# Optimization experiments

Hardware: AMD Instinct MI355X
Metric: run time of the kernel (lower is better)

The kernel has to match this reference:

```python
import jax, jax.numpy as jnp
import numpy as np

C = 128          # hidden_channels
H = 8            # num_heads
D = C // H       # head dim = 16
OUT = 64         # out_channels
L = 2            # num_layers
NN = (30000, 60000, 6000)                 # poi, road, region node counts
NE = (200000, 300000, 200000, 100000)     # edges per edge type
ETS = ((0, 1), (1, 1), (1, 2), (2, 0))    # (src_type, dst_type) per edge type


def setup_inputs():
    key = jax.random.key(0)
    ks = iter(jax.random.split(key, 40))
    s = 1.0 / np.sqrt(C)
    sd = 1.0 / np.sqrt(D)
    inp = {}
    inp['x_poi'] = jax.random.normal(next(ks), (NN[0], C), jnp.float32)
    inp['x_road'] = jax.random.normal(next(ks), (NN[1], C), jnp.float32)
    inp['x_region'] = jax.random.normal(next(ks), (NN[2], C), jnp.float32)
    for et, (si, di) in enumerate(ETS):
        inp[f'e{et}_src'] = jax.random.randint(next(ks), (NE[et],), 0, NN[si], jnp.int32)
        inp[f'e{et}_dst'] = jax.random.randint(next(ks), (NE[et],), 0, NN[di], jnp.int32)
    # per-node-type input projection
    inp['lin_w'] = jax.random.normal(next(ks), (3, C, C), jnp.float32) * s
    inp['lin_b'] = jax.random.normal(next(ks), (3, C), jnp.float32) * 0.01
    # per-layer, per-node-type K/Q/V and output projections
    for nm in ('kw', 'qw', 'vw', 'aw'):
        inp[nm] = jax.random.normal(next(ks), (L, 3, C, C), jnp.float32) * s
    for nm in ('kb', 'qb', 'vb', 'ab'):
        inp[nm] = jax.random.normal(next(ks), (L, 3, C), jnp.float32) * 0.01
    # per-layer, per-edge-type relation matrices and priors
    inp['a_rel'] = jax.random.normal(next(ks), (L, 4, H, D, D), jnp.float32) * sd
    inp['m_rel'] = jax.random.normal(next(ks), (L, 4, H, D, D), jnp.float32) * sd
    inp['p_rel'] = jnp.ones((L, 4, H), jnp.float32)
    inp['skip'] = jnp.ones((L, 3), jnp.float32)
    inp['out_w'] = jax.random.normal(next(ks), (C, OUT), jnp.float32) * s
    inp['out_b'] = jnp.zeros((OUT,), jnp.float32)
    return inp


def _seg_softmax(alpha, dst, n):
    amax = jax.lax.stop_gradient(jax.ops.segment_max(alpha, dst, num_segments=n))
    ex = jnp.exp(alpha - amax[dst])
    den = jax.ops.segment_sum(ex, dst, num_segments=n)
    return ex / (den[dst] + 1e-16)


def _hgt_forward(xs, edges, lin_w, lin_b, kw, kb, qw, qb, vw, vb, aw, ab,
                 a_rel, m_rel, p_rel, skip, out_w, out_b):
    # per-node-type input linear + relu
    xs = [jax.nn.relu(xs[i] @ lin_w[i] + lin_b[i]) for i in range(3)]
    scale = 1.0 / np.sqrt(D)
    for l in range(L):
        k = [(xs[i] @ kw[l, i] + kb[l, i]).reshape(-1, H, D) for i in range(3)]
        q = [(xs[i] @ qw[l, i] + qb[l, i]).reshape(-1, H, D) for i in range(3)]
        v = [(xs[i] @ vw[l, i] + vb[l, i]).reshape(-1, H, D) for i in range(3)]
        agg = [jnp.zeros((NN[i], H, D), xs[i].dtype) for i in range(3)]
        for et, (si, di) in enumerate(ETS):
            src, dst = edges[et]
            n = NN[di]
            ke = jnp.einsum('ehd,hdf->ehf', k[si][src], a_rel[l, et])   # [E,H,D]
            alpha = jnp.einsum('ehd,ehd->eh', q[di][dst], ke) * p_rel[l, et] * scale
            alpha = _seg_softmax(alpha, dst, n)                          # [E,H]
            m = jnp.einsum('ehd,hdf->ehf', v[si][src], m_rel[l, et])    # [E,H,D]
            agg[di] = agg[di] + jax.ops.segment_sum(m * alpha[..., None], dst, num_segments=n)
        new_xs = []
        for i in range(3):
            o = jax.nn.gelu(agg[i].reshape(-1, C)) @ aw[l, i] + ab[l, i]
            beta = jax.nn.sigmoid(skip[l, i])
            o = beta * o + (1.0 - beta) * xs[i]
            new_xs.append(jax.nn.relu(o))  # HGT applies activation after each conv
        xs = new_xs
    return (xs[0] @ out_w + out_b, xs[1] @ out_w + out_b, xs[2] @ out_w + out_b)


def reference(x_poi, x_road, x_region,
              e0_src, e0_dst, e1_src, e1_dst, e2_src, e2_dst, e3_src, e3_dst,
              lin_w, lin_b, kw, kb, qw, qb, vw, vb, aw, ab,
              a_rel, m_rel, p_rel, skip, out_w, out_b):
    edges = ((e0_src, e0_dst), (e1_src, e1_dst), (e2_src, e2_dst), (e3_src, e3_dst))
    return _hgt_forward([x_poi, x_road, x_region], edges,
                        lin_w, lin_b, kw, kb, qw, qb, vw, vb, aw, ab,
                        a_rel, m_rel, p_rel, skip, out_w, out_b)
```

## Files before the change

### kernel.cpp

```cpp
#include <hip/hip_runtime.h>
#include <cstddef>
#include <cstdint>


typedef __attribute__((ext_vector_type(8))) short short8;
typedef __attribute__((ext_vector_type(4))) float floatx4;

__device__ __forceinline__ float gelu_fast(float x) {
    float u = 1.5957691216057308f * x * (1.0f + 0.044715f * x * x);
    return x / (1.0f + __expf(-u));
}

__device__ __forceinline__ unsigned short f2bf(float f) {
    unsigned u = __float_as_uint(f);
    u += 0x7fffu + ((u >> 16) & 1);
    return (unsigned short)(u >> 16);
}

__device__ __forceinline__ float bf2f(unsigned short h) {
    return __uint_as_float((unsigned)h << 16);
}

__device__ __forceinline__ void up8(uint4 u, float* f) {
    f[0] = __uint_as_float(u.x << 16); f[1] = __uint_as_float(u.x & 0xffff0000u);
    f[2] = __uint_as_float(u.y << 16); f[3] = __uint_as_float(u.y & 0xffff0000u);
    f[4] = __uint_as_float(u.z << 16); f[5] = __uint_as_float(u.z & 0xffff0000u);
    f[6] = __uint_as_float(u.w << 16); f[7] = __uint_as_float(u.w & 0xffff0000u);
}

__device__ __forceinline__ uint4 pk8(const float* f) {
    uint4 u;
    u.x = (unsigned)f2bf(f[0]) | ((unsigned)f2bf(f[1]) << 16);
    u.y = (unsigned)f2bf(f[2]) | ((unsigned)f2bf(f[3]) << 16);
    u.z = (unsigned)f2bf(f[4]) | ((unsigned)f2bf(f[5]) << 16);
    u.w = (unsigned)f2bf(f[6]) | ((unsigned)f2bf(f[7]) << 16);
    return u;
}

__global__ __launch_bounds__(256, 2) void gemm_proj_all(
    const unsigned short* __restrict__ xs_bf,
    const unsigned short* __restrict__ Wl,
    const float* __restrict__ bl,
    unsigned short* __restrict__ proj)
{
    const int    NN_[3]  = {30000, 60000, 6000};
    const int    NPAN[3] = {469, 938, 94};
    const int    OFFr[3] = {0, 30000, 90000};
    const int    WOFF[3] = {0, 49152, 131072};
    const int    BOFF[3] = {0, 384, 1024};
    const size_t POFF[3] = {0, 11520000u, 49920000u};
    const int    LDO[3]  = {384, 640, 384};

    int b = blockIdx.x, t, cp, rb;
    if (b < 590)      { t = 1; cp = b / 118; rb = b - cp * 118; }
    else if (b < 767) { int lb = b - 590; t = 0; cp = lb / 59; rb = lb - cp * 59; }
    else              { int lb = b - 767; t = 2; cp = lb / 12; rb = lb - cp * 12; }
    int p0 = rb * 8, p1 = p0 + 8;
    if (p1 > NPAN[t]) p1 = NPAN[t];

    const unsigned short* Abf = xs_bf + (size_t)OFFr[t] * 128;
    const unsigned short* Wt  = Wl + WOFF[t];
    const float* bias = bl + BOFF[t] + cp * 128;
    unsigned short* outbf = proj + POFF[t];
    const int ldo = LDO[t], Nrows = NN_[t];

    const int wave = threadIdx.x >> 6, lane = threadIdx.x & 63;
    const int quad = lane >> 4, l16 = lane & 15;

    short8 B[2][4][4];
    {
        const unsigned short* wb = Wt + (size_t)(cp * 128 + l16) * 128 + quad * 8;
        #pragma unroll
        for (int T = 0; T < 2; ++T)
            #pragma unroll
            for (int c = 0; c < 4; ++c)
                #pragma unroll
                for (int kc = 0; kc < 4; ++kc)
                    B[T][c][kc] = *(const short8*)(wb + (size_t)(T * 64 + c * 16) * 128 + kc * 32);
    }
    float4 bv[2][4];
    #pragma unroll
    for (int T = 0; T < 2; ++T)
        #pragma unroll
        for (int c = 0; c < 4; ++c)
            bv[T][c] = *(const float4*)(bias + T * 64 + c * 16 + quad * 4);

    short8 Acur[4];
    {
        int m = p0 * 64 + wave * 16 + l16; if (m >= Nrows) m = Nrows - 1;
        const unsigned short* ap = Abf + (size_t)m * 128 + quad * 8;
        #pragma unroll
        for (int kc = 0; kc < 4; ++kc) Acur[kc] = *(const short8*)(ap + kc * 32);
    }
    for (int p = p0; p < p1; ++p) {
        short8 Anx[4];
        {
            int m = (p + 1) * 64 + wave * 16 + l16; if (m >= Nrows) m = Nrows - 1;
            const unsigned short* ap = Abf + (size_t)m * 128 + quad * 8;
            #pragma unroll
            for (int kc = 0; kc < 4; ++kc) Anx[kc] = *(const short8*)(ap + kc * 32);
        }
        floatx4 acc[2][4];
        #pragma unroll
        for (int T = 0; T < 2; ++T)
            #pragma unroll
            for (int c = 0; c < 4; ++c) acc[T][c] = (floatx4){0.f, 0.f, 0.f, 0.f};
        #pragma unroll
        for (int kc = 0; kc < 4; ++kc)
            #pragma unroll
            for (int T = 0; T < 2; ++T)
                #pragma unroll
                for (int c = 0; c < 4; ++c)
                    acc[T][c] = __builtin_amdgcn_mfma_f32_16x16x32_bf16(B[T][c][kc], Acur[kc], acc[T][c], 0, 0, 0);
        int node = p * 64 + wave * 16 + l16;
        if (node < Nrows) {
            unsigned short* op = outbf + (size_t)node * ldo + cp * 128 + quad * 4;
            #pragma unroll
            for (int T = 0; T < 2; ++T)
                #pragma unroll
                for (int c = 0; c < 4; ++c) {
                    uint2 u;
                    u.x = (unsigned)f2bf(acc[T][c][0] + bv[T][c].x) |
                          ((unsigned)f2bf(acc[T][c][1] + bv[T][c].y) << 16);
                    u.y = (unsigned)f2bf(acc[T][c][2] + bv[T][c].z) |
                          ((unsigned)f2bf(acc[T][c][3] + bv[T][c].w) << 16);
                    *(uint2*)(op + T * 64 + c * 16) = u;
                }
        }
        #pragma unroll
        for (int kc = 0; kc < 4; ++kc) Acur[kc] = Anx[kc];
    }
}

template<bool AF32, bool GIN, bool SKIP>
__global__ __launch_bounds__(256, 2) void gemm_node(
    const void* __restrict__ a0v, const void* __restrict__ a1v, const void* __restrict__ a2v,
    const unsigned short* __restrict__ WtB, const float* __restrict__ biasB,
    const unsigned short* __restrict__ xoldB, const float* __restrict__ skipB,
    unsigned short* __restrict__ outB)
{
    const int TN[3]   = {30000, 60000, 6000};
    const int NPAN[3] = {469, 938, 94};
    const int TOFF[3] = {0, 30000, 90000};
    int b = blockIdx.x, t, rb;
    if (b < 235)      { t = 0; rb = b; }
    else if (b < 704) { t = 1; rb = b - 235; }
    else              { t = 2; rb = b - 704; }
    int p0 = rb * 2, p1 = p0 + 2;
    if (p1 > NPAN[t]) p1 = NPAN[t];
    int Nrows = TN[t];
    const void* av = (t == 0) ? a0v : (t == 1) ? a1v : a2v;
    const unsigned short* xold = xoldB + (size_t)TOFF[t] * 128;
    unsigned short* out = outB + (size_t)TOFF[t] * 128;

    const int wave = threadIdx.x >> 6, lane = threadIdx.x & 63;
    const int quad = lane >> 4, l16 = lane & 15;

    short8 B[8][4];
    {
        const unsigned short* wb = WtB + (size_t)t * 16384 + (size_t)l16 * 128 + quad * 8;
        #pragma unroll
        for (int c = 0; c < 8; ++c)
            #pragma unroll
            for (int kc = 0; kc < 4; ++kc)
                B[c][kc] = *(const short8*)(wb + (size_t)c * 2048 + kc * 32);
    }
    float beta = 0.f, omb = 0.f;
    if (SKIP) { beta = 1.0f / (1.0f + __expf(-skipB[t])); omb = 1.0f - beta; }

    short8 Acur[4];
    {
        int m = p0 * 64 + wave * 16 + l16; if (m >= Nrows) m = Nrows - 1;
        size_t base = (size_t)m * 128 + quad * 8;
        #pragma unroll
        for (int kc = 0; kc < 4; ++kc) {
            if (AF32) {
                const float* ap = (const float*)av + base;
                float4 f0 = *(const float4*)(ap + kc * 32);
                float4 f1 = *(const float4*)(ap + kc * 32 + 4);
                float af[8] = {f0.x, f0.y, f0.z, f0.w, f1.x, f1.y, f1.z, f1.w};
                short8 a;
                #pragma unroll
                for (int i = 0; i < 8; ++i) a[i] = (short)f2bf(af[i]);
                Acur[kc] = a;
            } else if (GIN) {
                const unsigned short* ap = (const unsigned short*)av + base;
                short8 a8 = *(const short8*)(ap + kc * 32);
                short8 a;
                #pragma unroll
                for (int i = 0; i < 8; ++i)
                    a[i] = (short)f2bf(gelu_fast(bf2f((unsigned short)a8[i])));
                Acur[kc] = a;
            } else {
                const unsigned short* ap = (const unsigned short*)av + base;
                Acur[kc] = *(const short8*)(ap + kc * 32);
            }
        }
    }
    for (int p = p0; p < p1; ++p) {
        float4 Fnx[4][2];
        short8 Snx[4];
        {
            int m = (p + 1) * 64 + wave * 16 + l16; if (m >= Nrows) m = Nrows - 1;
            size_t base = (size_t)m * 128 + quad * 8;
            #pragma unroll
            for (int kc = 0; kc < 4; ++kc) {
                if (AF32) {
                    const float* ap = (const float*)av + base;
                    Fnx[kc][0] = *(const float4*)(ap + kc * 32);
                    Fnx[kc][1] = *(const float4*)(ap + kc * 32 + 4);
                } else {
                    const unsigned short* ap = (const unsigned short*)av + base;
                    Snx[kc] = *(const short8*)(ap + kc * 32);
                }
            }
        }
        int node = p * 64 + wave * 16 + l16;
        int ncl = (node < Nrows) ? node : (Nrows - 1);
        uint2 xo[8];
        if (SKIP) {
            #pragma unroll
            for (int c = 0; c < 8; ++c)
                xo[c] = *(const uint2*)(xold + (size_t)ncl * 128 + c * 16 + quad * 4);
        }
        floatx4 acc[8];
        #pragma unroll
        for (int c = 0; c < 8; ++c) acc[c] = (floatx4){0.f, 0.f, 0.f, 0.f};
        #pragma unroll
        for (int kc = 0; kc < 4; ++kc)
            #pragma unroll
            for (int c = 0; c < 8; ++c)
                acc[c] = __builtin_amdgcn_mfma_f32_16x16x32_bf16(B[c][kc], Acur[kc], acc[c], 0, 0, 0);
        if (node < Nrows) {
            #pragma unroll
            for (int c = 0; c < 8; ++c) {
                int col0 = c * 16 + quad * 4;
                float4 bv = *(const float4*)(biasB + t * 128 + col0);
                float o0 = acc[c][0] + bv.x, o1 = acc[c][1] + bv.y;
                float o2 = acc[c][2] + bv.z, o3 = acc[c][3] + bv.w;
                if (SKIP) {
                    o0 = beta * o0 + omb * __uint_as_float(xo[c].x << 16);
                    o1 = beta * o1 + omb * __uint_as_float(xo[c].x & 0xffff0000u);
                    o2 = beta * o2 + omb * __uint_as_float(xo[c].y << 16);
                    o3 = beta * o3 + omb * __uint_as_float(xo[c].y & 0xffff0000u);
                }
                o0 = fmaxf(o0, 0.f); o1 = fmaxf(o1, 0.f);
                o2 = fmaxf(o2, 0.f); o3 = fmaxf(o3, 0.f);
                uint2 u;
                u.x = (unsigned)f2bf(o0) | ((unsigned)f2bf(o1) << 16);
                u.y = (unsigned)f2bf(o2) | ((unsigned)f2bf(o3) << 16);
                *(uint2*)(out + (size_t)node * 128 + col0) = u;
            }
        }
        #pragma unroll
        for (int kc = 0; kc < 4; ++kc) {
            if (AF32) {
                float af[8] = {Fnx[kc][0].x, Fnx[kc][0].y, Fnx[kc][0].z, Fnx[kc][0].w,
                               Fnx[kc][1].x, Fnx[kc][1].y, Fnx[kc][1].z, Fnx[kc][1].w};
                short8 a;
                #pragma unroll
                for (int i = 0; i < 8; ++i) a[i] = (short)f2bf(af[i]);
                Acur[kc] = a;
            } else if (GIN) {
                short8 a;
                #pragma unroll
                for (int i = 0; i < 8; ++i)
                    a[i] = (short)f2bf(gelu_fast(bf2f((unsigned short)Snx[kc][i])));
                Acur[kc] = a;
            } else {
                Acur[kc] = Snx[kc];
            }
        }
    }
}

__global__ __launch_bounds__(256, 3) void gemm_out(
    const unsigned short* __restrict__ Abf,
    const unsigned short* __restrict__ Wt,
    const float* __restrict__ bias,
    float* __restrict__ out, int Nrows)
{
    const int wave = threadIdx.x >> 6, lane = threadIdx.x & 63;
    const int quad = lane >> 4, l16 = lane & 15;
    int p0 = blockIdx.x * 4, p1 = p0 + 4;

    short8 B[4][4];
    {
        const unsigned short* wb = Wt + (size_t)l16 * 128 + quad * 8;
        #pragma unroll
        for (int c = 0; c < 4; ++c)
            #pragma unroll
            for (int kc = 0; kc < 4; ++kc)
                B[c][kc] = *(const short8*)(wb + (size_t)c * 2048 + kc * 32);
    }
    float4 bv[4];
    #pragma unroll
    for (int c = 0; c < 4; ++c) bv[c] = *(const float4*)(bias + c * 16 + quad * 4);

    short8 Acur[4];
    {
        int m = p0 * 64 + wave * 16 + l16; if (m >= Nrows) m = Nrows - 1;
        const unsigned short* ap = Abf + (size_t)m * 128 + quad * 8;
        #pragma unroll
        for (int kc = 0; kc < 4; ++kc) Acur[kc] = *(const short8*)(ap + kc * 32);
    }
    for (int p = p0; p < p1; ++p) {
        short8 Anx[4];
        {
            int m = (p + 1) * 64 + wave * 16 + l16; if (m >= Nrows) m = Nrows - 1;
            const unsigned short* ap = Abf + (size_t)m * 128 + quad * 8;
            #pragma unroll
            for (int kc = 0; kc < 4; ++kc) Anx[kc] = *(const short8*)(ap + kc * 32);
        }
        floatx4 acc[4];
        #pragma unroll
        for (int c = 0; c < 4; ++c) acc[c] = (floatx4){0.f, 0.f, 0.f, 0.f};
        #pragma unroll
        for (int kc = 0; kc < 4; ++kc)
            #pragma unroll
            for (int c = 0; c < 4; ++c)
                acc[c] = __builtin_amdgcn_mfma_f32_16x16x32_bf16(B[c][kc], Acur[kc], acc[c], 0, 0, 0);
        int node = p * 64 + wave * 16 + l16;
        if (node < Nrows) {
            #pragma unroll
            for (int c = 0; c < 4; ++c) {
                float4 o;
                o.x = acc[c][0] + bv[c].x; o.y = acc[c][1] + bv[c].y;
                o.z = acc[c][2] + bv[c].z; o.w = acc[c][3] + bv[c].w;
                *(float4*)(out + (size_t)node * 64 + c * 16 + quad * 4) = o;
            }
        }
        #pragma unroll
        for (int kc = 0; kc < 4; ++kc) Acur[kc] = Anx[kc];
    }
}

__global__ __launch_bounds__(128) void prep_qpack(
    const float* __restrict__ qw, const float* __restrict__ qb,
    unsigned short* __restrict__ Wpack, float* __restrict__ bpack)
{
    const int pre[3] = {0, 49152, 131072};
    const int preB[3] = {0, 384, 1024};
    int n = threadIdx.x, k = blockIdx.x, t = blockIdx.y, l = blockIdx.z;
    unsigned short* Wp = Wpack + (size_t)l * 180224 + pre[t];
    Wp[(size_t)n * 128 + k] = f2bf(qw[(size_t)(l * 3 + t) * 16384 + (size_t)k * 128 + n]);
    if (k == 0) bpack[l * 1408 + preB[t] + n] = qb[(l * 3 + t) * 128 + n];
}

__global__ __launch_bounds__(128) void fold_rel_pack(
    const float* __restrict__ kw, const float* __restrict__ kb,
    const float* __restrict__ vw, const float* __restrict__ vb,
    const float* __restrict__ a_rel, const float* __restrict__ m_rel,
    unsigned short* __restrict__ Wpack, float* __restrict__ bpack)
{
    const int SIv[4] = {0, 1, 1, 2};
    const int SLOT[4] = {0, 0, 1, 0};
    const int pre[3] = {0, 49152, 131072};
    const int preB[3] = {0, 384, 1024};
    int hf = threadIdx.x, h = hf >> 4, f = hf & 15;
    int c = blockIdx.x, et = blockIdx.y, l = blockIdx.z;
    int si = SIv[et];
    const float* kwp  = kw + (size_t)(l * 3 + si) * 16384;
    const float* vwp  = vw + (size_t)(l * 3 + si) * 16384;
    const float* kbp  = kb + (size_t)(l * 3 + si) * 128;
    const float* vbp  = vb + (size_t)(l * 3 + si) * 128;
    const float* arel = a_rel + (size_t)(l * 4 + et) * 2048;
    const float* mrel = m_rel + (size_t)(l * 4 + et) * 2048;
    float sk = 0.f, sv = 0.f;
    #pragma unroll
    for (int d = 0; d < 16; ++d) {
        float ar = arel[(h * 16 + d) * 16 + f];
        float mr = mrel[(h * 16 + d) * 16 + f];
        sk = fmaf(kwp[c * 128 + h * 16 + d], ar, sk);
        sv = fmaf(vwp[c * 128 + h * 16 + d], mr, sv);
    }
    int rowoff = 128 + 256 * SLOT[et];
    unsigned short* Wp = Wpack + (size_t)l * 180224 + pre[si];
    Wp[(size_t)(rowoff + hf) * 128 + c]       = f2bf(sk);
    Wp[(size_t)(rowoff + 128 + hf) * 128 + c] = f2bf(sv);
    if (c == 0) {
        float bk = 0.f, bvv = 0.f;
        #pragma unroll
        for (int d = 0; d < 16; ++d) {
            bk  = fmaf(kbp[h * 16 + d], arel[(h * 16 + d) * 16 + f], bk);
            bvv = fmaf(vbp[h * 16 + d], mrel[(h * 16 + d) * 16 + f], bvv);
        }
        float* bp = bpack + l * 1408 + preB[si];
        bp[rowoff + hf]       = bk;
        bp[rowoff + 128 + hf] = bvv;
    }
}

__global__ __launch_bounds__(128) void prep_w9(
    const float* __restrict__ lin_w, const float* __restrict__ aw,
    unsigned short* __restrict__ lwt, unsigned short* __restrict__ awt)
{
    int n = threadIdx.x, k = blockIdx.x, mi = blockIdx.y;
    const float* w; unsigned short* wt; int m;
    if (mi < 3) { w = lin_w; wt = lwt; m = mi; }
    else        { w = aw;    wt = awt; m = mi - 3; }
    wt[(size_t)m * 16384 + (size_t)n * 128 + k] =
        f2bf(w[(size_t)m * 16384 + (size_t)k * 128 + n]);
}

__global__ __launch_bounds__(64) void prep_owt(
    const float* __restrict__ ow, unsigned short* __restrict__ owt)
{
    int n = threadIdx.x, k = blockIdx.x;
    owt[(size_t)n * 128 + k] = f2bf(ow[(size_t)k * 64 + n]);
}

__global__ __launch_bounds__(256) void hist_all(
    const int* __restrict__ d0, const int* __restrict__ d1,
    const int* __restrict__ d2, const int* __restrict__ d3,
    int* __restrict__ deg4)
{
    const int Ev[4] = {200000, 300000, 200000, 100000};
    int et = blockIdx.y;
    int e = blockIdx.x * 256 + threadIdx.x;
    if (e >= Ev[et]) return;
    const int* d = et == 0 ? d0 : et == 1 ? d1 : et == 2 ? d2 : d3;
    atomicAdd(&deg4[et * 60000 + d[e]], 1);
}

__global__ __launch_bounds__(256) void scan_tile_all(
    const int* __restrict__ deg4,
    int* __restrict__ r0, int* __restrict__ r1, int* __restrict__ r2, int* __restrict__ r3,
    int* __restrict__ tsum4)
{
    const int Ndv[4] = {60000, 60000, 6000, 30000};
    __shared__ int ls[256];
    int et = blockIdx.y;
    int n = Ndv[et];
    const int* deg = deg4 + et * 60000;
    int* rowptr = et == 0 ? r0 : et == 1 ? r1 : et == 2 ? r2 : r3;
    int b = blockIdx.x, tid = threadIdx.x;
    int base = b * 1024 + tid * 4;
    int v0 = 0, v1 = 0, v2 = 0, v3 = 0;
    if (base + 3 < n) {
        int4 t = *(const int4*)(deg + base);
        v0 = t.x; v1 = t.y; v2 = t.z; v3 = t.w;
    } else {
        if (base + 0 < n) v0 = deg[base + 0];
        if (base + 1 < n) v1 = deg[base + 1];
        if (base + 2 < n) v2 = deg[base + 2];
        if (base + 3 < n) v3 = deg[base + 3];
    }
    int s = v0 + v1 + v2 + v3;
    ls[tid] = s;
    __syncthreads();
    #pragma unroll
    for (int off = 1; off < 256; off <<= 1) {
        int t = (tid >= off) ? ls[tid - off] : 0;
        __syncthreads();
        ls[tid] += t;
        __syncthreads();
    }
    int run = ls[tid] - s;
    int o0 = run; run += v0;
    int o1 = run; run += v1;
    int o2 = run; run += v2;
    int o3 = run;
    if (base + 3 < n) {
        *(int4*)(rowptr + base) = make_int4(o0, o1, o2, o3);
    } else {
        if (base + 0 < n) rowptr[base + 0] = o0;
        if (base + 1 < n) rowptr[base + 1] = o1;
        if (base + 2 < n) rowptr[base + 2] = o2;
    }
    if (tid == 255) tsum4[et * 64 + b] = ls[255];
}

__global__ __launch_bounds__(64) void scan_tsum_all(
    int* __restrict__ tsum4,
    int* __restrict__ r0, int* __restrict__ r1, int* __restrict__ r2, int* __restrict__ r3)
{
    const int Ndv[4] = {60000, 60000, 6000, 30000};
    int et = blockIdx.x;
    int n = Ndv[et];
    int nt = (n + 1023) >> 10;
    int* tileSum = tsum4 + et * 64;
    int* rowptr = et == 0 ? r0 : et == 1 ? r1 : et == 2 ? r2 : r3;
    int tid = threadIdx.x;
    int v = (tid < nt) ? tileSum[tid] : 0;
    int orig = v;
    #pragma unroll
    for (int off = 1; off < 64; off <<= 1) {
        int t = __shfl_up(v, off);
        if (tid >= off) v += t;
    }
    if (tid < nt) tileSum[tid] = v - orig;
    if (tid == nt - 1) rowptr[n] = v;
}

__global__ __launch_bounds__(256) void scan_add_all(
    int* __restrict__ r0, int* __restrict__ r1, int* __restrict__ r2, int* __restrict__ r3,
    const int* __restrict__ tsum4)
{
    const int Ndv[4] = {60000, 60000, 6000, 30000};
    int et = blockIdx.y;
    int n = Ndv[et];
    int* rowptr = et == 0 ? r0 : et == 1 ? r1 : et == 2 ? r2 : r3;
    int i = blockIdx.x * 256 + threadIdx.x;
    if (i < n) rowptr[i] += tsum4[et * 64 + (i >> 10)];
}

__global__ __launch_bounds__(256) void fill_all(
    const int* __restrict__ s0, const int* __restrict__ d0,
    const int* __restrict__ s1, const int* __restrict__ d1,
    const int* __restrict__ s2, const int* __restrict__ d2,
    const int* __restrict__ s3, const int* __restrict__ d3,
    const int* __restrict__ r0, const int* __restrict__ r1,
    const int* __restrict__ r2, const int* __restrict__ r3,
    int* __restrict__ deg4,
    int* __restrict__ c0, int* __restrict__ c1, int* __restrict__ c2, int* __restrict__ c3)
{
    const int Ev[4] = {200000, 300000, 200000, 100000};
    int et = blockIdx.y;
    int e = blockIdx.x * 256 + threadIdx.x;
    if (e >= Ev[et]) return;
    const int* src = et == 0 ? s0 : et == 1 ? s1 : et == 2 ? s2 : s3;
    const int* dst = et == 0 ? d0 : et == 1 ? d1 : et == 2 ? d2 : d3;
    const int* rowptr = et == 0 ? r0 : et == 1 ? r1 : et == 2 ? r2 : r3;
    int* csr = et == 0 ? c0 : et == 1 ? c1 : et == 2 ? c2 : c3;
    int d = dst[e];
    int pos = atomicAdd(&deg4[et * 60000 + d], 1);
    csr[rowptr[d] + pos] = src[e];
}

__device__ __forceinline__ void attn_run(
    const int* __restrict__ csr, int beg, int end,
    const unsigned short* __restrict__ kbase, int ld,
    const float* qf, float ph, float& m, float& l, float* o)
{
    if (beg >= end) return;
    int s = csr[beg];
    const uint4* kp = (const uint4*)(kbase + (size_t)s * ld);
    uint4 ku0 = kp[0], ku1 = kp[1];
    uint4 vu0 = kp[16], vu1 = kp[17];
    for (int j = beg; j < end; ++j) {
        uint4 nk0 = ku0, nk1 = ku1, nv0 = vu0, nv1 = vu1;
        if (j + 1 < end) {
            int sn = csr[j + 1];
            const uint4* np = (const uint4*)(kbase + (size_t)sn * ld);
            nk0 = np[0]; nk1 = np[1]; nv0 = np[16]; nv1 = np[17];
        }
        float kf[16], vf[16];
        up8(ku0, kf); up8(ku1, kf + 8);
        up8(vu0, vf); up8(vu1, vf + 8);
        float a = 0.f;
        #pragma unroll
        for (int i = 0; i < 16; ++i) a = fmaf(qf[i], kf[i], a);
        a *= ph;
        float d = a - m;
        if (d > 8.f) {
            float sc = __expf(-d);
            l *= sc;
            #pragma unroll
            for (int i = 0; i < 16; ++i) o[i] *= sc;
            m = a; d = 0.f;
        }
        float w = __expf(d);
        l += w;
        #pragma unroll
        for (int i = 0; i < 16; ++i) o[i] = fmaf(w, vf[i], o[i]);
        ku0 = nk0; ku1 = nk1; vu0 = nv0; vu1 = nv1;
    }
}

__global__ __launch_bounds__(256) void agg_all(
    const int* __restrict__ rp0, const int* __restrict__ cs0,
    const int* __restrict__ rp1, const int* __restrict__ cs1,
    const int* __restrict__ rp2, const int* __restrict__ cs2,
    const int* __restrict__ rp3, const int* __restrict__ cs3,
    const unsigned short* __restrict__ P0, const unsigned short* __restrict__ P1,
    const unsigned short* __restrict__ P2,
    const float* __restrict__ prl,
    unsigned short* __restrict__ num)
{
    int gb = blockIdx.x, tid = threadIdx.x;
    float qf[16], o[16], r[16];
    if (gb < 1875) {
        int t = gb * 256 + tid;
        int node = t >> 3, h = t & 7;
        const uint4* qp = (const uint4*)(P1 + (size_t)node * 640 + h * 16);
        up8(qp[0], qf); up8(qp[1], qf + 8);
        float m0 = -INFINITY, l0 = 0.f;
        #pragma unroll
        for (int i = 0; i < 16; ++i) o[i] = 0.f;
        attn_run(cs0, rp0[node], rp0[node + 1], P0 + 128 + h * 16, 384,
                 qf, prl[h] * 0.25f, m0, l0, o);
        float i0 = 1.f / (l0 + 1e-16f);
        #pragma unroll
        for (int i = 0; i < 16; ++i) { r[i] = i0 * o[i]; o[i] = 0.f; }
        float m1 = -INFINITY, l1 = 0.f;
        attn_run(cs1, rp1[node], rp1[node + 1], P1 + 128 + h * 16, 640,
                 qf, prl[8 + h] * 0.25f, m1, l1, o);
        float i1 = 1.f / (l1 + 1e-16f);
        #pragma unroll
        for (int i = 0; i < 16; ++i) r[i] += i1 * o[i];
        uint4* np = (uint4*)(num + (size_t)(30000 + node) * 128 + h * 16);
        np[0] = pk8(r); np[1] = pk8(r + 8);
    } else if (gb < 2625) {
        int t = (gb - 1875) * 256 + tid;
        int node = t >> 5, h = t & 7, sub = (t >> 3) & 3;
        int beg0 = rp2[node], end0 = rp2[node + 1];
        int n = end0 - beg0;
        int beg = beg0 + ((n * sub) >> 2);
        int end = beg0 + ((n * (sub + 1)) >> 2);
        const uint4* qp = (const uint4*)(P2 + (size_t)node * 384 + h * 16);
        up8(qp[0], qf); up8(qp[1], qf + 8);
        float m = -INFINITY, l = 0.f;
        #pragma unroll
        for (int i = 0; i < 16; ++i) o[i] = 0.f;
        attn_run(cs2, beg, end, P1 + 384 + h * 16, 640,
                 qf, prl[16 + h] * 0.25f, m, l, o);
        #pragma unroll
        for (int st = 8; st <= 16; st <<= 1) {
            float mp = __shfl_xor(m, st);
            float lp = __shfl_xor(l, st);
            float mn = fmaxf(m, mp);
            float sc  = (l  > 0.f) ? __expf(m  - mn) : 0.f;
            float scp = (lp > 0.f) ? __expf(mp - mn) : 0.f;
            l = l * sc + lp * scp;
            #pragma unroll
            for (int i = 0; i < 16; ++i) {
                float op = __shfl_xor(o[i], st);
                o[i] = o[i] * sc + op * scp;
            }
            m = mn;
        }
        if (sub) return;
        float inv = 1.f / (l + 1e-16f);
        #pragma unroll
        for (int i = 0; i < 16; ++i) r[i] = inv * o[i];
        uint4* np = (uint4*)(num + (size_t)(90000 + node) * 128 + h * 16);
        np[0] = pk8(r); np[1] = pk8(r + 8);
    } else {
        int t = (gb - 2625) * 256 + tid;
        if (t >= 240000) return;
        int node = t >> 3, h = t & 7;
        const uint4* qp = (const uint4*)(P0 + (size_t)node * 384 + h * 16);
        up8(qp[0], qf); up8(qp[1], qf + 8);
        float m = -INFINITY, l = 0.f;
        #pragma unroll
        for (int i = 0; i < 16; ++i) o[i] = 0.f;
        attn_run(cs3, rp3[node], rp3[node + 1], P2 + 128 + h * 16, 384,
                 qf, prl[24 + h] * 0.25f, m, l, o);
        float inv = 1.f / (l + 1e-16f);
        #pragma unroll
        for (int i = 0; i < 16; ++i) r[i] = inv * o[i];
        uint4* np = (uint4*)(num + (size_t)node * 128 + h * 16);
        np[0] = pk8(r); np[1] = pk8(r + 8);
    }
}

extern "C" void kernel_launch(void* const* d_in, const int* in_sizes, int n_in,
                              void* d_out, int out_size, void* d_ws, size_t ws_size,
                              hipStream_t stream)
{
    (void)in_sizes; (void)n_in; (void)out_size; (void)ws_size;

    const float* xin[3] = {(const float*)d_in[0], (const float*)d_in[1], (const float*)d_in[2]};
    const int* esrc[4] = {(const int*)d_in[3], (const int*)d_in[5], (const int*)d_in[7], (const int*)d_in[9]};
    const int* edst[4] = {(const int*)d_in[4], (const int*)d_in[6], (const int*)d_in[8], (const int*)d_in[10]};
    const float* lin_w = (const float*)d_in[11];
    const float* lin_b = (const float*)d_in[12];
    const float* kw = (const float*)d_in[13];
    const float* qw = (const float*)d_in[14];
    const float* vw = (const float*)d_in[15];
    const float* aw = (const float*)d_in[16];
    const float* kb = (const float*)d_in[17];
    const float* qb = (const float*)d_in[18];
    const float* vb = (const float*)d_in[19];
    const float* ab = (const float*)d_in[20];
    const float* a_rel = (const float*)d_in[21];
    const float* m_rel = (const float*)d_in[22];
    const float* p_rel = (const float*)d_in[23];
    const float* skip  = (const float*)d_in[24];
    const float* out_w = (const float*)d_in[25];
    const float* out_b = (const float*)d_in[26];

    float* ws = (float*)d_ws;
    unsigned short* num   = (unsigned short*)ws;
    unsigned short* xs_bf = (unsigned short*)(ws + 6144000);
    unsigned short* proj  = (unsigned short*)(ws + 12288000);
    unsigned short* Wpack = (unsigned short*)(ws + 38400000);
    unsigned short* lwt   = (unsigned short*)(ws + 38580224);
    unsigned short* awt   = (unsigned short*)(ws + 38604800);
    unsigned short* owt   = (unsigned short*)(ws + 38653952);
    float*          bpack = ws + 38658048;
    int*            deg4  = (int*)(ws + 38660864);
    int*            tsum4 = (int*)(ws + 38900864);
    int* rp[4];
    rp[0] = (int*)(ws + 38901120);
    rp[1] = (int*)(ws + 38961128);
    rp[2] = (int*)(ws + 39021136);
    rp[3] = (int*)(ws + 39027144);
    int* cs[4];
    cs[0] = (int*)(ws + 39057152);
    cs[1] = (int*)(ws + 39257152);
    cs[2] = (int*)(ws + 39557152);
    cs[3] = (int*)(ws + 39757152);

    unsigned short* P[3];
    P[0] = proj;
    P[1] = proj + (size_t)30000 * 384;
    P[2] = proj + (size_t)30000 * 384 + (size_t)60000 * 640;

    dim3 blk(256);

    hipMemsetAsync(deg4, 0, 960000, stream);
    hist_all<<<dim3(1172, 4), blk, 0, stream>>>(edst[0], edst[1], edst[2], edst[3], deg4);
    scan_tile_all<<<dim3(59, 4), blk, 0, stream>>>(deg4, rp[0], rp[1], rp[2], rp[3], tsum4);
    scan_tsum_all<<<dim3(4), dim3(64), 0, stream>>>(tsum4, rp[0], rp[1], rp[2], rp[3]);
    scan_add_all<<<dim3(235, 4), blk, 0, stream>>>(rp[0], rp[1], rp[2], rp[3], tsum4);
    hipMemsetAsync(deg4, 0, 960000, stream);
    fill_all<<<dim3(1172, 4), blk, 0, stream>>>(
        esrc[0], edst[0], esrc[1], edst[1], esrc[2], edst[2], esrc[3], edst[3],
        rp[0], rp[1], rp[2], rp[3], deg4, cs[0], cs[1], cs[2], cs[3]);

    prep_qpack<<<dim3(128, 3, 2), dim3(128), 0, stream>>>(qw, qb, Wpack, bpack);
    fold_rel_pack<<<dim3(128, 4, 2), dim3(128), 0, stream>>>(
        kw, kb, vw, vb, a_rel, m_rel, Wpack, bpack);
    prep_w9<<<dim3(128, 9), dim3(128), 0, stream>>>(lin_w, aw, lwt, awt);
    prep_owt<<<dim3(128), dim3(64), 0, stream>>>(out_w, owt);

    gemm_node<true, false, false><<<dim3(751), blk, 0, stream>>>(
        xin[0], xin[1], xin[2], lwt, lin_b, nullptr, nullptr, xs_bf);

    for (int l = 0; l < 2; ++l) {
        gemm_proj_all<<<dim3(803), blk, 0, stream>>>(
            xs_bf, Wpack + (size_t)l * 180224, bpack + l * 1408, proj);

        agg_all<<<dim3(3563), blk, 0, stream>>>(
            rp[0], cs[0], rp[1], cs[1], rp[2], cs[2], rp[3], cs[3],
            P[0], P[1], P[2], p_rel + (size_t)l * 32, num);

        gemm_node<false, true, true><<<dim3(751), blk, 0, stream>>>(
            num, num + (size_t)30000 * 128, num + (size_t)90000 * 128,
            awt + (size_t)l * 3 * 16384, ab + (size_t)l * 3 * 128,
            xs_bf, skip + l * 3, xs_bf);
    }

    gemm_out<<<dim3(375), blk, 0, stream>>>(
        xs_bf, owt, out_b, (float*)d_out, 96000);
}
```

Measured before the change: 580.6 us.

## Sort destination nodes by degree for load balance and unroll edge loop by two

Adds a counting-sort pass (histogram, scan, scatter) that builds per-node-type permutations of destination nodes ordered by in-degree. The aggregation kernel then looks nodes up through these permutations, so warps hold nodes of similar degree and diverge less. The online-softmax edge loop is also reworked to handle two edges per iteration with two-ahead prefetch of K/V rows. The cost is three small extra kernels, an indirection on node index, and scattered output writes.

```diff
diff --git a/kernel.cpp b/kernel.cpp
--- a/kernel.cpp
+++ b/kernel.cpp
@@ -528,43 +528,140 @@
     csr[rowptr[d] + pos] = src[e];
 }
 
+__global__ __launch_bounds__(256) void perm_hist(
+    const int* __restrict__ rp0, const int* __restrict__ rp1,
+    const int* __restrict__ rp2, const int* __restrict__ rp3,
+    int* __restrict__ hist)
+{
+    const int N[3] = {60000, 30000, 6000};
+    int sec = blockIdx.y;
+    int i = blockIdx.x * 256 + threadIdx.x;
+    if (i >= N[sec]) return;
+    int d;
+    if (sec == 0)      d = (rp0[i + 1] - rp0[i]) + (rp1[i + 1] - rp1[i]);
+    else if (sec == 1) d = rp3[i + 1] - rp3[i];
+    else               d = rp2[i + 1] - rp2[i];
+    atomicAdd(&hist[sec * 512 + (d < 511 ? d : 511)], 1);
+}
+
+__global__ __launch_bounds__(512) void perm_scan(int* __restrict__ hist)
+{
+    __shared__ int ls[512];
+    int* h = hist + blockIdx.x * 512;
+    int tid = threadIdx.x;
+    int v = h[tid];
+    ls[tid] = v;
+    __syncthreads();
+    for (int off = 1; off < 512; off <<= 1) {
+        int t = (tid >= off) ? ls[tid - off] : 0;
+        __syncthreads();
+        ls[tid] += t;
+        __syncthreads();
+    }
+    h[tid] = ls[tid] - v;
+}
+
+__global__ __launch_bounds__(256) void perm_scatter(
+    const int* __restrict__ rp0, const int* __restrict__ rp1,
+    const int* __restrict__ rp2, const int* __restrict__ rp3,
+    int* __restrict__ hist,
+    int* __restrict__ permR, int* __restrict__ permP, int* __restrict__ permG)
+{
+    const int N[3] = {60000, 30000, 6000};
+    int sec = blockIdx.y;
+    int i = blockIdx.x * 256 + threadIdx.x;
+    if (i >= N[sec]) return;
+    int d;
+    if (sec == 0)      d = (rp0[i + 1] - rp0[i]) + (rp1[i + 1] - rp1[i]);
+    else if (sec == 1) d = rp3[i + 1] - rp3[i];
+    else               d = rp2[i + 1] - rp2[i];
+    int pos = atomicAdd(&hist[sec * 512 + (d < 511 ? d : 511)], 1);
+    int* perm = (sec == 0) ? permR : (sec == 1) ? permP : permG;
+    perm[pos] = i;
+}
+
+__device__ __forceinline__ void attn_edge(
+    uint4 k0, uint4 k1, uint4 v0, uint4 v1,
+    const float* qf, float ph, float& m, float& l, float* o)
+{
+    float kf[16];
+    up8(k0, kf); up8(k1, kf + 8);
+    float a = 0.f;
+    #pragma unroll
+    for (int i = 0; i < 16; ++i) a = fmaf(qf[i], kf[i], a);
+    a *= ph;
+    float d = a - m;
+    if (d > 8.f) {
+        float sc = __expf(-d);
+        l *= sc;
+        #pragma unroll
+        for (int i = 0; i < 16; ++i) o[i] *= sc;
+        m = a; d = 0.f;
+    }
+    float w = __expf(d);
+    l += w;
+    float vf[16];
+    up8(v0, vf); up8(v1, vf + 8);
+    #pragma unroll
+    for (int i = 0; i < 16; ++i) o[i] = fmaf(w, vf[i], o[i]);
+}
+
 __device__ __forceinline__ void attn_run(
     const int* __restrict__ csr, int beg, int end,
     const unsigned short* __restrict__ kbase, int ld,
     const float* qf, float ph, float& m, float& l, float* o)
 {
-    if (beg >= end) return;
-    int s = csr[beg];
-    const uint4* kp = (const uint4*)(kbase + (size_t)s * ld);
-    uint4 ku0 = kp[0], ku1 = kp[1];
-    uint4 vu0 = kp[16], vu1 = kp[17];
-    for (int j = beg; j < end; ++j) {
-        uint4 nk0 = ku0, nk1 = ku1, nv0 = vu0, nv1 = vu1;
-        if (j + 1 < end) {
-            int sn = csr[j + 1];
-            const uint4* np = (const uint4*)(kbase + (size_t)sn * ld);
-            nk0 = np[0]; nk1 = np[1]; nv0 = np[16]; nv1 = np[17];
-        }
-        float kf[16], vf[16];
-        up8(ku0, kf); up8(ku1, kf + 8);
-        up8(vu0, vf); up8(vu1, vf + 8);
-        float a = 0.f;
-        #pragma unroll
-        for (int i = 0; i < 16; ++i) a = fmaf(qf[i], kf[i], a);
-        a *= ph;
-        float d = a - m;
+    int n = end - beg;
+    if (n <= 0) return;
+    const uint4* pA = (const uint4*)(kbase + (size_t)csr[beg] * ld);
+    uint4 A0 = pA[0], A1 = pA[1], A2 = pA[16], A3 = pA[17];
+    uint4 B0 = A0, B1 = A1, B2 = A2, B3 = A3;
+    if (n > 1) {
+        const uint4* pB = (const uint4*)(kbase + (size_t)csr[beg + 1] * ld);
+        B0 = pB[0]; B1 = pB[1]; B2 = pB[16]; B3 = pB[17];
+    }
+    int j = beg;
+    for (; j + 3 < end; j += 2) {
+        const uint4* pC = (const uint4*)(kbase + (size_t)csr[j + 2] * ld);
+        const uint4* pD = (const uint4*)(kbase + (size_t)csr[j + 3] * ld);
+        uint4 C0 = pC[0], C1 = pC[1], C2 = pC[16], C3 = pC[17];
+        uint4 D0 = pD[0], D1 = pD[1], D2 = pD[16], D3 = pD[17];
+        float kf0[16], kf1[16];
+        up8(A0, kf0); up8(A1, kf0 + 8);
+        up8(B0, kf1); up8(B1, kf1 + 8);
+        float a0 = 0.f, a1 = 0.f;
+        #pragma unroll
+        for (int i = 0; i < 16; ++i) {
+            a0 = fmaf(qf[i], kf0[i], a0);
+            a1 = fmaf(qf[i], kf1[i], a1);
+        }
+        a0 *= ph; a1 *= ph;
+        float hi = fmaxf(a0, a1);
+        float d = hi - m;
         if (d > 8.f) {
             float sc = __expf(-d);
             l *= sc;
             #pragma unroll
             for (int i = 0; i < 16; ++i) o[i] *= sc;
-            m = a; d = 0.f;
-        }
-        float w = __expf(d);
-        l += w;
-        #pragma unroll
-        for (int i = 0; i < 16; ++i) o[i] = fmaf(w, vf[i], o[i]);
-        ku0 = nk0; ku1 = nk1; vu0 = nv0; vu1 = nv1;
+            m = hi;
+        }
+        float w0 = __expf(a0 - m), w1 = __expf(a1 - m);
+        l += w0 + w1;
+        float vf0[16], vf1[16];
+        up8(A2, vf0); up8(A3, vf0 + 8);
+        up8(B2, vf1); up8(B3, vf1 + 8);
+        #pragma unroll
+        for (int i = 0; i < 16; ++i)
+            o[i] = fmaf(w1, vf1[i], fmaf(w0, vf0[i], o[i]));
+        A0 = C0; A1 = C1; A2 = C2; A3 = C3;
+        B0 = D0; B1 = D1; B2 = D2; B3 = D3;
+    }
+    int rem = end - j;
+    attn_edge(A0, A1, A2, A3, qf, ph, m, l, o);
+    if (rem >= 2) attn_edge(B0, B1, B2, B3, qf, ph, m, l, o);
+    if (rem == 3) {
+        const uint4* pC = (const uint4*)(kbase + (size_t)csr[j + 2] * ld);
+        attn_edge(pC[0], pC[1], pC[16], pC[17], qf, ph, m, l, o);
     }
 }
 
@@ -576,13 +673,15 @@
     const unsigned short* __restrict__ P0, const unsigned short* __restrict__ P1,
     const unsigned short* __restrict__ P2,
     const float* __restrict__ prl,
+    const int* __restrict__ pmR, const int* __restrict__ pmP,
+    const int* __restrict__ pmG,
     unsigned short* __restrict__ num)
 {
     int gb = blockIdx.x, tid = threadIdx.x;
     float qf[16], o[16], r[16];
     if (gb < 1875) {
         int t = gb * 256 + tid;
-        int node = t >> 3, h = t & 7;
+        int node = pmR[t >> 3], h = t & 7;
         const uint4* qp = (const uint4*)(P1 + (size_t)node * 640 + h * 16);
         up8(qp[0], qf); up8(qp[1], qf + 8);
         float m0 = -INFINITY, l0 = 0.f;
@@ -603,7 +702,7 @@
         np[0] = pk8(r); np[1] = pk8(r + 8);
     } else if (gb < 2625) {
         int t = (gb - 1875) * 256 + tid;
-        int node = t >> 5, h = t & 7, sub = (t >> 3) & 3;
+        int node = pmG[t >> 5], h = t & 7, sub = (t >> 3) & 3;
         int beg0 = rp2[node], end0 = rp2[node + 1];
         int n = end0 - beg0;
         int beg = beg0 + ((n * sub) >> 2);
@@ -639,7 +738,7 @@
     } else {
         int t = (gb - 2625) * 256 + tid;
         if (t >= 240000) return;
-        int node = t >> 3, h = t & 7;
+        int node = pmP[t >> 3], h = t & 7;
         const uint4* qp = (const uint4*)(P0 + (size_t)node * 384 + h * 16);
         up8(qp[0], qf); up8(qp[1], qf + 8);
         float m = -INFINITY, l = 0.f;
@@ -702,6 +801,10 @@
     cs[1] = (int*)(ws + 39257152);
     cs[2] = (int*)(ws + 39557152);
     cs[3] = (int*)(ws + 39757152);
+    int* permR = deg4;
+    int* permP = deg4 + 60000;
+    int* permG = deg4 + 90000;
+    int* phist = deg4 + 96000;
 
     unsigned short* P[3];
     P[0] = proj;
@@ -720,6 +823,12 @@
         esrc[0], edst[0], esrc[1], edst[1], esrc[2], edst[2], esrc[3], edst[3],
         rp[0], rp[1], rp[2], rp[3], deg4, cs[0], cs[1], cs[2], cs[3]);
 
+    hipMemsetAsync(phist, 0, 1536 * 4, stream);
+    perm_hist<<<dim3(235, 3), blk, 0, stream>>>(rp[0], rp[1], rp[2], rp[3], phist);
+    perm_scan<<<dim3(3), dim3(512), 0, stream>>>(phist);
+    perm_scatter<<<dim3(235, 3), blk, 0, stream>>>(
+        rp[0], rp[1], rp[2], rp[3], phist, permR, permP, permG);
+
     prep_qpack<<<dim3(128, 3, 2), dim3(128), 0, stream>>>(qw, qb, Wpack, bpack);
     fold_rel_pack<<<dim3(128, 4, 2), dim3(128), 0, stream>>>(
         kw, kb, vw, vb, a_rel, m_rel, Wpack, bpack);
@@ -735,7 +844,8 @@
 
         agg_all<<<dim3(3563), blk, 0, stream>>>(
             rp[0], cs[0], rp[1], cs[1], rp[2], cs[2], rp[3], cs[3],
-            P[0], P[1], P[2], p_rel + (size_t)l * 32, num);
+            P[0], P[1], P[2], p_rel + (size_t)l * 32,
+            permR, permP, permG, num);
 
         gemm_node<false, true, true><<<dim3(751), blk, 0, stream>>>(
             num, num + (size_t)30000 * 128, num + (size_t)90000 * 128,
```

New measurement: 1.022 ms. +76.1%, slower.
